# Optimization experiments

Measured on AMD Instinct MI355X. Metric: run time of the kernel, lower is better.

Reference implementation:

```python
import jax, jax.numpy as jnp
import numpy as np

RADIUS = 4.0

def _gather(x, idx):
    # x: [b, C, N], idx: [b, n, k] -> out: [b, C, k, n]
    b, C, N = x.shape
    _, n, k = idx.shape
    idxT = jnp.broadcast_to(idx.transpose(0, 2, 1)[:, None, :, :], (b, C, k, n))
    return jnp.take_along_axis(x[:, :, None, :], idxT, axis=3)


def setup_inputs() -> dict:
    key = jax.random.key(0)
    k1, k2, k3, k4, k5, k6 = jax.random.split(key, 6)
    b, N, k = 2, 50000, 16
    c_in, c_out, K = 64, 128, 5
    c2 = c_out // 2
    xyz = jax.random.normal(k1, (b, 3, N), dtype=jnp.float32)
    fea = jax.random.normal(k2, (b, c_in, N), dtype=jnp.float32)
    knn_idx = jax.random.randint(k3, (b, N, k), 0, N)
    conv_w = jax.random.normal(k4, (c2, c_in), dtype=jnp.float32) * 0.05
    conv_b = jax.random.normal(k5, (c2,), dtype=jnp.float32) * 0.01
    # uniform init matching torch: bound = sqrt(3)*gain/sqrt(fan), gain=sqrt(2), fan=16
    bound = float(np.sqrt(3.0) * np.sqrt(2.0) / np.sqrt(16.0))
    conv_dw = jax.random.uniform(k6, (1, c2, K, K, K), dtype=jnp.float32, minval=-bound, maxval=bound)
    return {"xyz": xyz, "fea": fea, "knn_idx": knn_idx, "conv_w": conv_w, "conv_b": conv_b, "conv_dw": conv_dw}


def reference(xyz, fea, knn_idx, conv_w, conv_b, conv_dw):
    b, n, k = knn_idx.shape
    K = conv_dw.shape[-1]
    # --- geometry: gather neighbor coords, relative coords, normalize ---
    neighbor_xyz = _gather(xyz, knn_idx)            # [b, 3, k, n]
    rel = neighbor_xyz - xyz[:, :, None, :]         # [b, 3, k, n]
    std = jnp.std(rel, axis=(2, 3), keepdims=True, ddof=1)  # torch unbiased std
    sample = rel / (RADIUS * std)                   # normalized grid coords in channel dim
    # --- features: residual gather (center + neighbor diffs), 1x1 conv ---
    center = fea[:, :, None, :]                     # [b, C, 1, n]
    nb = _gather(fea, knn_idx[:, :, 1:])            # [b, C, k-1, n]
    nfea = jnp.concatenate([center, nb - center], axis=2)  # [b, C, k, n]
    nfea = jnp.einsum('oc,bckn->bokn', conv_w, nfea) + conv_b[None, :, None, None]
    # --- grid_sample(mode='nearest', padding='border', align_corners=False) ---
    def to_idx(coord):
        ix = ((coord + 1.0) * K - 1.0) * 0.5
        return jnp.clip(jnp.round(ix), 0, K - 1).astype(jnp.int32)
    ix = to_idx(sample[:, 0])  # grid x -> W index, [b, k, n]
    iy = to_idx(sample[:, 1])  # grid y -> H index
    iz = to_idx(sample[:, 2])  # grid z -> D index
    kern = conv_dw[0][:, iz, iy, ix]                # [C2, b, k, n]
    kern = jnp.transpose(kern, (1, 0, 2, 3))        # [b, C2, k, n]
    # --- weighted reduce over neighbors + mean branch ---
    out = jnp.concatenate([(kern * nfea).sum(axis=2), nfea.mean(axis=2)], axis=1)
    return out  # [b, out_channels, n]
```

## Files before the change

### kernel.cpp

```cpp
#include <hip/hip_runtime.h>
#include <hip/hip_bf16.h>
#include <math.h>

#define NPTS 50000
#define BATCH 2
#define CIN 64
#define C2 64
#define KNN 16
#define NCELL 125
#define MTOT 800000


using bf16x8 = __attribute__((ext_vector_type(8))) short;
using f32x4  = __attribute__((ext_vector_type(4))) float;
using f32x2  = __attribute__((ext_vector_type(2))) float;

__device__ __forceinline__ f32x2 unpk(unsigned int v) {
    f32x2 r;
    r.x = __uint_as_float(v << 16);
    r.y = __uint_as_float(v & 0xffff0000u);
    return r;
}
__device__ __forceinline__ unsigned short f2bf(float f) {
    __hip_bfloat16 h = __float2bfloat16(f);
    return *(unsigned short*)&h;
}

__device__ __forceinline__ int to_cell32(float s) {
    float x = __fmul_rn(__fsub_rn(__fmul_rn(__fadd_rn(s, 1.0f), 5.0f), 1.0f), 0.5f);
    x = rintf(x);
    x = fminf(fmaxf(x, 0.0f), 4.0f);
    return (int)x;
}

__device__ __forceinline__ void leafwalk(int l, int& off, int& n) {
    off = 0; n = 25000;
    #pragma unroll
    for (int d = 7; d >= 0; --d) {
        int n2 = (n >> 1); n2 -= (n2 & 7);
        if ((l >> d) & 1) { off += n2; n -= n2; } else { n = n2; }
    }
}

__global__ __launch_bounds__(256) void kprep(const float* __restrict__ xyz,
                                             const float* __restrict__ dw,
                                             float* __restrict__ wsf) {
    int bx = blockIdx.x;
    int t = threadIdx.x;
    if (bx < 391) {
        int gid = bx * 256 + t;
        if (gid < 2 * NPTS) {
            int b = (gid >= NPTS);
            int n = gid - b * NPTS;
            const float* xb = xyz + (size_t)b * 3 * NPTS;
            float3 v;
            v.x = xb[n]; v.y = xb[NPTS + n]; v.z = xb[2 * NPTS + n];
            ((float3*)(wsf + 16384))[gid] = v;
        }
    } else {
        unsigned int* gdwp = (unsigned int*)(wsf + 8192);
        int i0 = (bx - 391) * 250;
        for (int i = i0 + t; i < i0 + 250; i += 256) {
            int cell = i >> 5, u = i & 31;
            unsigned int p0 = f2bf(dw[(2 * u)     * NCELL + cell]);
            unsigned int p1 = f2bf(dw[(2 * u + 1) * NCELL + cell]);
            gdwp[i] = p0 | (p1 << 16);
        }
    }
}

__global__ __launch_bounds__(256) void kfuse1(const int* __restrict__ knn,
                                              const float* __restrict__ fea,
                                              const float* __restrict__ W,
                                              unsigned short* __restrict__ g,
                                              float3* __restrict__ rel3,
                                              float* __restrict__ wsf) {
    __shared__ unsigned short flds[64 * 72];
    int bx = blockIdx.x;
    int t = threadIdx.x;
    if (bx < 1564) {
        int b = (bx >= 782);
        int tile = bx - b * 782;
        int n0 = tile * 64;
        int nrem = NPTS - n0; if (nrem > 64) nrem = 64;
        const float* fb = fea + (size_t)b * CIN * NPTS;
        int j = t & 63, w = t >> 6;
        int lane = t & 63, li = lane & 15, gq = lane >> 4;
        #pragma unroll
        for (int i = 0; i < 8; ++i) {
            int c = w * 2 + i * 8;
            float v0 = (j < nrem) ? fb[(size_t)c * NPTS + n0 + j] : 0.0f;
            float v1 = (j < nrem) ? fb[(size_t)(c + 1) * NPTS + n0 + j] : 0.0f;
            unsigned int pk = (unsigned int)f2bf(v0) | ((unsigned int)f2bf(v1) << 16);
            *(unsigned int*)&flds[j * 72 + c] = pk;
        }
        bf16x8 af[4][2];
        #pragma unroll
        for (int mt = 0; mt < 4; ++mt)
            #pragma unroll
            for (int kh = 0; kh < 2; ++kh) {
                const float* wp = W + (mt * 16 + li) * CIN + kh * 32 + gq * 8;
                float4 wa = *(const float4*)wp;
                float4 wb = *(const float4*)(wp + 4);
                bf16x8 a;
                a[0] = (short)f2bf(wa.x); a[1] = (short)f2bf(wa.y);
                a[2] = (short)f2bf(wa.z); a[3] = (short)f2bf(wa.w);
                a[4] = (short)f2bf(wb.x); a[5] = (short)f2bf(wb.y);
                a[6] = (short)f2bf(wb.z); a[7] = (short)f2bf(wb.w);
                af[mt][kh] = a;
            }
        __syncthreads();
        f32x4 acc[4];
        #pragma unroll
        for (int mt = 0; mt < 4; ++mt) acc[mt] = (f32x4){0.f, 0.f, 0.f, 0.f};
        #pragma unroll
        for (int kh = 0; kh < 2; ++kh) {
            bf16x8 bfv = *(const bf16x8*)&flds[(w * 16 + li) * 72 + kh * 32 + gq * 8];
            #pragma unroll
            for (int mt = 0; mt < 4; ++mt)
                acc[mt] = __builtin_amdgcn_mfma_f32_16x16x32_bf16(af[mt][kh], bfv,
                                                                  acc[mt], 0, 0, 0);
        }
        int nloc = w * 16 + li;
        if (nloc < nrem) {
            unsigned short* gr = g + ((size_t)b * NPTS + n0 + nloc) * C2;
            #pragma unroll
            for (int mt = 0; mt < 4; ++mt) {
                int ob = mt * 16 + gq * 4;
                uint2 pk;
                pk.x = (unsigned int)f2bf(acc[mt][0]) | ((unsigned int)f2bf(acc[mt][1]) << 16);
                pk.y = (unsigned int)f2bf(acc[mt][2]) | ((unsigned int)f2bf(acc[mt][3]) << 16);
                *(uint2*)(gr + ob) = pk;
            }
        }
    } else {
        float* lsum = (float*)flds;
        const float3* xyzT = (const float3*)(wsf + 16384);
        int pid = bx - 1564;
        int b = pid >> 8, r8 = pid & 255;
        int s = r8 >> 3, blk = r8 & 7;
        const float3* xT = xyzT + (size_t)b * NPTS;
        const int* kb = knn + (size_t)b * NPTS * KNN;
        float3* relb = rel3 + (size_t)b * MTOT;
        int l = blk * 32 + (t >> 3);
        int j = t & 7;
        int off, n;
        leafwalk(l, off, n);
        int base = s * 25000 + off;
        float r0 = 0.0f, r1 = 0.0f, r2 = 0.0f;
        int i = j;
        for (; i + 24 < n; i += 32) {
            int f0 = base + i, f1 = f0 + 8, f2 = f0 + 16, f3 = f0 + 24;
            int kk0 = f0 / NPTS, nn0 = f0 - kk0 * NPTS;
            int kk1 = f1 / NPTS, nn1 = f1 - kk1 * NPTS;
            int kk2 = f2 / NPTS, nn2 = f2 - kk2 * NPTS;
            int kk3 = f3 / NPTS, nn3 = f3 - kk3 * NPTS;
            int jA = kb[nn0 * KNN + kk0];
            int jB = kb[nn1 * KNN + kk1];
            int jC = kb[nn2 * KNN + kk2];
            int jD = kb[nn3 * KNN + kk3];
            float3 cA = xT[nn0], nA = xT[jA];
            float3 cB = xT[nn1], nB = xT[jB];
            float3 cC = xT[nn2], nC = xT[jC];
            float3 cD = xT[nn3], nD = xT[jD];
            float3 vA, vB, vC, vD;
            vA.x = __fsub_rn(nA.x, cA.x); vA.y = __fsub_rn(nA.y, cA.y); vA.z = __fsub_rn(nA.z, cA.z);
            vB.x = __fsub_rn(nB.x, cB.x); vB.y = __fsub_rn(nB.y, cB.y); vB.z = __fsub_rn(nB.z, cB.z);
            vC.x = __fsub_rn(nC.x, cC.x); vC.y = __fsub_rn(nC.y, cC.y); vC.z = __fsub_rn(nC.z, cC.z);
            vD.x = __fsub_rn(nD.x, cD.x); vD.y = __fsub_rn(nD.y, cD.y); vD.z = __fsub_rn(nD.z, cD.z);
            relb[f0] = vA; relb[f1] = vB; relb[f2] = vC; relb[f3] = vD;
            r0 = __fadd_rn(r0, vA.x); r1 = __fadd_rn(r1, vA.y); r2 = __fadd_rn(r2, vA.z);
            r0 = __fadd_rn(r0, vB.x); r1 = __fadd_rn(r1, vB.y); r2 = __fadd_rn(r2, vB.z);
            r0 = __fadd_rn(r0, vC.x); r1 = __fadd_rn(r1, vC.y); r2 = __fadd_rn(r2, vC.z);
            r0 = __fadd_rn(r0, vD.x); r1 = __fadd_rn(r1, vD.y); r2 = __fadd_rn(r2, vD.z);
        }
        for (; i < n; i += 8) {
            int f = base + i;
            int kk = f / NPTS, nn = f - kk * NPTS;
            int jj = kb[nn * KNN + kk];
            float3 cc = xT[nn], nv = xT[jj];
            float3 v;
            v.x = __fsub_rn(nv.x, cc.x); v.y = __fsub_rn(nv.y, cc.y); v.z = __fsub_rn(nv.z, cc.z);
            relb[f] = v;
            r0 = __fadd_rn(r0, v.x); r1 = __fadd_rn(r1, v.y); r2 = __fadd_rn(r2, v.z);
        }
        float a0 = __fadd_rn(r0, __shfl_xor(r0, 1));
        a0 = __fadd_rn(a0, __shfl_xor(a0, 2));
        a0 = __fadd_rn(a0, __shfl_xor(a0, 4));
        float a1 = __fadd_rn(r1, __shfl_xor(r1, 1));
        a1 = __fadd_rn(a1, __shfl_xor(a1, 2));
        a1 = __fadd_rn(a1, __shfl_xor(a1, 4));
        float a2 = __fadd_rn(r2, __shfl_xor(r2, 1));
        a2 = __fadd_rn(a2, __shfl_xor(a2, 2));
        a2 = __fadd_rn(a2, __shfl_xor(a2, 4));
        #pragma unroll
        for (int c = 0; c < 3; ++c) {
            float rc = (c == 0) ? a0 : ((c == 1) ? a1 : a2);
            __syncthreads();
            if (j == 0) lsum[t >> 3] = rc;
            __syncthreads();
            for (int m = 16; m >= 1; m >>= 1) {
                float v = 0.0f;
                if (t < m) v = __fadd_rn(lsum[2 * t], lsum[2 * t + 1]);
                __syncthreads();
                if (t < m) lsum[t] = v;
                __syncthreads();
            }
            if (t == 0) wsf[16 + ((size_t)(b * 3 + c) * 32 + s) * 8 + blk] = lsum[0];
        }
    }
}

__global__ __launch_bounds__(256) void kpw2(const float3* __restrict__ rel3,
                                            float* __restrict__ wsf) {
    __shared__ float sm[96];
    int r8 = blockIdx.x;
    int s = r8 >> 3, blk = r8 & 7;
    int b = blockIdx.y;
    int t = threadIdx.x;

    if (t < 96) {
        int c = t >> 5, l = t & 31;
        const float* q = wsf + 16 + (size_t)(b * 3 + c) * 256 + l * 8;
        float a  = __fadd_rn(__fadd_rn(q[0], q[1]), __fadd_rn(q[2], q[3]));
        float b2 = __fadd_rn(__fadd_rn(q[4], q[5]), __fadd_rn(q[6], q[7]));
        sm[c * 32 + l] = __fadd_rn(a, b2);
    }
    __syncthreads();
    for (int m = 16; m >= 1; m >>= 1) {
        float v = 0.0f;
        int c = t >> 5, l = t & 31;
        if (t < 96 && l < m) v = __fadd_rn(sm[c * 32 + 2 * l], sm[c * 32 + 2 * l + 1]);
        __syncthreads();
        if (t < 96 && l < m) sm[c * 32 + l] = v;
        __syncthreads();
    }
    float m0 = sm[0]  / 800000.0f;
    float m1 = sm[32] / 800000.0f;
    float m2 = sm[64] / 800000.0f;
    __syncthreads();

    const float3* relb = rel3 + (size_t)b * MTOT;
    int l = blk * 32 + (t >> 3);
    int j = t & 7;
    int off, n;
    leafwalk(l, off, n);
    int base = s * 25000 + off;
    float r0 = 0.0f, r1 = 0.0f, r2 = 0.0f;
    int i = j;
    for (; i + 24 < n; i += 32) {
        float3 vA = relb[base + i];
        float3 vB = relb[base + i + 8];
        float3 vC = relb[base + i + 16];
        float3 vD = relb[base + i + 24];
        float dA0 = __fsub_rn(vA.x, m0), dA1 = __fsub_rn(vA.y, m1), dA2 = __fsub_rn(vA.z, m2);
        float dB0 = __fsub_rn(vB.x, m0), dB1 = __fsub_rn(vB.y, m1), dB2 = __fsub_rn(vB.z, m2);
        float dC0 = __fsub_rn(vC.x, m0), dC1 = __fsub_rn(vC.y, m1), dC2 = __fsub_rn(vC.z, m2);
        float dD0 = __fsub_rn(vD.x, m0), dD1 = __fsub_rn(vD.y, m1), dD2 = __fsub_rn(vD.z, m2);
        r0 = __fadd_rn(r0, __fmul_rn(dA0, dA0));
        r1 = __fadd_rn(r1, __fmul_rn(dA1, dA1));
        r2 = __fadd_rn(r2, __fmul_rn(dA2, dA2));
        r0 = __fadd_rn(r0, __fmul_rn(dB0, dB0));
        r1 = __fadd_rn(r1, __fmul_rn(dB1, dB1));
        r2 = __fadd_rn(r2, __fmul_rn(dB2, dB2));
        r0 = __fadd_rn(r0, __fmul_rn(dC0, dC0));
        r1 = __fadd_rn(r1, __fmul_rn(dC1, dC1));
        r2 = __fadd_rn(r2, __fmul_rn(dC2, dC2));
        r0 = __fadd_rn(r0, __fmul_rn(dD0, dD0));
        r1 = __fadd_rn(r1, __fmul_rn(dD1, dD1));
        r2 = __fadd_rn(r2, __fmul_rn(dD2, dD2));
    }
    for (; i < n; i += 8) {
        float3 v = relb[base + i];
        float d0 = __fsub_rn(v.x, m0), d1 = __fsub_rn(v.y, m1), d2 = __fsub_rn(v.z, m2);
        r0 = __fadd_rn(r0, __fmul_rn(d0, d0));
        r1 = __fadd_rn(r1, __fmul_rn(d1, d1));
        r2 = __fadd_rn(r2, __fmul_rn(d2, d2));
    }
    float a0 = __fadd_rn(r0, __shfl_xor(r0, 1));
    a0 = __fadd_rn(a0, __shfl_xor(a0, 2));
    a0 = __fadd_rn(a0, __shfl_xor(a0, 4));
    float a1 = __fadd_rn(r1, __shfl_xor(r1, 1));
    a1 = __fadd_rn(a1, __shfl_xor(a1, 2));
    a1 = __fadd_rn(a1, __shfl_xor(a1, 4));
    float a2 = __fadd_rn(r2, __shfl_xor(r2, 1));
    a2 = __fadd_rn(a2, __shfl_xor(a2, 2));
    a2 = __fadd_rn(a2, __shfl_xor(a2, 4));
    #pragma unroll
    for (int c = 0; c < 3; ++c) {
        float rc = (c == 0) ? a0 : ((c == 1) ? a1 : a2);
        __syncthreads();
        if (j == 0) sm[t >> 3] = rc;
        __syncthreads();
        for (int m = 16; m >= 1; m >>= 1) {
            float v = 0.0f;
            if (t < m) v = __fadd_rn(sm[2 * t], sm[2 * t + 1]);
            __syncthreads();
            if (t < m) sm[t] = v;
            __syncthreads();
        }
        if (t == 0) wsf[2048 + ((size_t)(b * 3 + c) * 32 + s) * 8 + blk] = sm[0];
    }
}

__global__ __launch_bounds__(256, 6) void kmain(const int* __restrict__ idx,
                                                const float* __restrict__ cb,
                                                const unsigned short* __restrict__ g,
                                                const float* __restrict__ wsf,
                                                float* __restrict__ out) {
    __shared__ unsigned int  dwp[NCELL * 32];
    __shared__ unsigned char celllds[64 * KNN];
    __shared__ float         ctr[3][64];
    __shared__ float         res[128 * 17];
    int bx = blockIdx.x;
    int sub = bx & 7;
    int b = sub >> 2;
    int tile = (bx >> 3) * 4 + (sub & 3);
    if (tile >= 782) return;
    int n0 = tile * 64;
    int t = threadIdx.x;
    int nrem = NPTS - n0; if (nrem > 64) nrem = 64;

    float* l3 = res;
    if (t < 96) {
        int c = t >> 5, l = t & 31;
        const float* q = wsf + 2048 + (size_t)(b * 3 + c) * 256 + l * 8;
        float a  = __fadd_rn(__fadd_rn(q[0], q[1]), __fadd_rn(q[2], q[3]));
        float b2 = __fadd_rn(__fadd_rn(q[4], q[5]), __fadd_rn(q[6], q[7]));
        l3[c * 32 + l] = __fadd_rn(a, b2);
    }
    __syncthreads();
    for (int m = 16; m >= 1; m >>= 1) {
        float v = 0.0f;
        int c = t >> 5, l = t & 31;
        if (t < 96 && l < m) v = __fadd_rn(l3[c * 32 + 2 * l], l3[c * 32 + 2 * l + 1]);
        __syncthreads();
        if (t < 96 && l < m) l3[c * 32 + l] = v;
        __syncthreads();
    }
    float dn0 = __fmul_rn(4.0f, sqrtf(l3[0]  / 799999.0f));
    float dn1 = __fmul_rn(4.0f, sqrtf(l3[32] / 799999.0f));
    float dn2 = __fmul_rn(4.0f, sqrtf(l3[64] / 799999.0f));
    __syncthreads();

    const unsigned int* gdwp = (const unsigned int*)(wsf + 8192);
    for (int i = t; i < NCELL * 32; i += 256) dwp[i] = gdwp[i];
    const float3* xT = (const float3*)(wsf + 16384) + (size_t)b * NPTS;
    if (t < 64) {
        if (t < nrem) {
            float3 v = xT[n0 + t];
            ctr[0][t] = v.x; ctr[1][t] = v.y; ctr[2][t] = v.z;
        }
    }
    const int* ib = idx + ((size_t)b * NPTS + n0) * KNN;
    __syncthreads();

    for (int i = t; i < nrem * KNN; i += 256) {
        int p = i >> 4;
        int jx = ib[i];
        float3 pj = xT[jx];
        float sx = __fsub_rn(pj.x, ctr[0][p]) / dn0;
        float sy = __fsub_rn(pj.y, ctr[1][p]) / dn1;
        float sz = __fsub_rn(pj.z, ctr[2][p]) / dn2;
        celllds[i] = (unsigned char)((to_cell32(sz) * 5 + to_cell32(sy)) * 5 + to_cell32(sx));
    }
    __syncthreads();

    int w = t >> 6, h = (t >> 5) & 1, u = t & 31;
    int o0 = 2 * u, o1 = 2 * u + 1;
    f32x2 cbv;
    cbv.x = cb[o0]; cbv.y = cb[o1];
    const unsigned short* gbp = g + (size_t)b * NPTS * C2;
    float* ob = out + (size_t)b * 128 * NPTS;

    #pragma unroll 1
    for (int chunk = 0; chunk < 4; ++chunk) {
        int pbase = chunk * 16;
        #pragma unroll 1
        for (int i = 0; i < 2; ++i) {
            int p = pbase + i * 8 + w * 2 + h;
            if (p < nrem) {
                const int* row = ib + p * KNN;
                unsigned int gnu = *(const unsigned int*)(gbp + (size_t)(n0 + p) * C2 + o0);
                unsigned int gvv[15];
                #pragma unroll
                for (int k = 0; k < 15; ++k) {
                    int jj = row[k + 1];
                    gvv[k] = *(const unsigned int*)(gbp + (size_t)jj * C2 + o0);
                }
                int cell0 = celllds[p * KNN];
                f32x2 k0v = unpk(dwp[cell0 * 32 + u]);
                f32x2 gn  = unpk(gnu);
                f32x2 ws = {0.f, 0.f}, gs = {0.f, 0.f}, sk = {0.f, 0.f};
                #pragma unroll
                for (int k = 0; k < 15; ++k) {
                    int cell = celllds[p * KNN + k + 1];
                    f32x2 dp = unpk(dwp[cell * 32 + u]);
                    f32x2 gv = unpk(gvv[k]);
                    ws += dp * gv;
                    gs += gv;
                    sk += dp;
                }
                f32x2 r1 = cbv * (k0v + sk) + gn * (k0v - sk) + ws;
                f32x2 r2 = cbv + 0.0625f * (gs - 14.0f * gn);
                int pl = p & 15;
                res[o0 * 17 + pl]        = r1.x;
                res[o1 * 17 + pl]        = r1.y;
                res[(64 + o0) * 17 + pl] = r2.x;
                res[(64 + o1) * 17 + pl] = r2.y;
            }
        }
        __syncthreads();
        int rl = t >> 4;
        int jn = t & 15;
        int ncol = nrem - pbase; if (ncol > 16) ncol = 16;
        if (jn < ncol) {
            for (int r2 = rl; r2 < 128; r2 += 16)
                ob[(size_t)r2 * NPTS + n0 + pbase + jn] = res[r2 * 17 + jn];
        }
        __syncthreads();
    }
}

extern "C" void kernel_launch(void* const* d_in, const int* in_sizes, int n_in,
                              void* d_out, int out_size, void* d_ws, size_t ws_size,
                              hipStream_t stream) {
    const float* xyz   = (const float*)d_in[0];
    const float* fea   = (const float*)d_in[1];
    const int*   knn   = (const int*)d_in[2];
    const float* convw = (const float*)d_in[3];
    const float* convb = (const float*)d_in[4];
    const float* convdw= (const float*)d_in[5];
    float* out = (float*)d_out;
    float* wsf = (float*)d_ws;
    unsigned short* g = (unsigned short*)(wsf + 327680);
    float3* rel3 = (float3*)out;

    kprep <<<407, 256, 0, stream>>>(xyz, convdw, wsf);
    kfuse1<<<1564 + 512, 256, 0, stream>>>(knn, fea, convw, g, rel3, wsf);
    kpw2  <<<dim3(256, BATCH), 256, 0, stream>>>(rel3, wsf);
    kmain <<<1568, 256, 0, stream>>>(knn, convb, g, wsf, out);
}
```

Measured before the change: 99.51 us.

## Split cell computation into separate kernel and halve channels per main block

Moves the per-neighbor grid-cell index computation out of the main kernel into a new kcell kernel that writes byte cell indices to workspace. The main kernel now splits the 64 output channels into two halves across blocks, so each block stages half the depthwise weight table in LDS and holds a smaller result buffer, allowing higher occupancy (launch bound 8) and twice as many blocks. Each block processes four points per wave per chunk instead of two serial iterations, and output writes use nontemporal stores. The cost is an extra kernel launch, a global round-trip for the cell bytes, and the knn index rows being read twice, once by each half.

New measurement: 103.9 us. 4.4% more time.

```diff
diff --git a/kernel.cpp b/kernel.cpp
--- a/kernel.cpp
+++ b/kernel.cpp
@@ -303,25 +303,16 @@
     }
 }
 
-__global__ __launch_bounds__(256, 6) void kmain(const int* __restrict__ idx,
-                                                const float* __restrict__ cb,
-                                                const unsigned short* __restrict__ g,
-                                                const float* __restrict__ wsf,
-                                                float* __restrict__ out) {
-    __shared__ unsigned int  dwp[NCELL * 32];
-    __shared__ unsigned char celllds[64 * KNN];
-    __shared__ float         ctr[3][64];
-    __shared__ float         res[128 * 17];
-    int bx = blockIdx.x;
-    int sub = bx & 7;
-    int b = sub >> 2;
-    int tile = (bx >> 3) * 4 + (sub & 3);
-    if (tile >= 782) return;
+__global__ __launch_bounds__(256) void kcell(const int* __restrict__ idx,
+                                             const float* __restrict__ wsf,
+                                             unsigned char* __restrict__ cells) {
+    __shared__ float l3[96];
+    __shared__ float ctr[3][64];
+    int tile = blockIdx.x, b = blockIdx.y;
     int n0 = tile * 64;
     int t = threadIdx.x;
     int nrem = NPTS - n0; if (nrem > 64) nrem = 64;
 
-    float* l3 = res;
     if (t < 96) {
         int c = t >> 5, l = t & 31;
         const float* q = wsf + 2048 + (size_t)(b * 3 + c) * 256 + l * 8;
@@ -341,20 +332,16 @@
     float dn0 = __fmul_rn(4.0f, sqrtf(l3[0]  / 799999.0f));
     float dn1 = __fmul_rn(4.0f, sqrtf(l3[32] / 799999.0f));
     float dn2 = __fmul_rn(4.0f, sqrtf(l3[64] / 799999.0f));
-    __syncthreads();
-
-    const unsigned int* gdwp = (const unsigned int*)(wsf + 8192);
-    for (int i = t; i < NCELL * 32; i += 256) dwp[i] = gdwp[i];
+
     const float3* xT = (const float3*)(wsf + 16384) + (size_t)b * NPTS;
-    if (t < 64) {
-        if (t < nrem) {
-            float3 v = xT[n0 + t];
-            ctr[0][t] = v.x; ctr[1][t] = v.y; ctr[2][t] = v.z;
-        }
+    if (t < 64 && t < nrem) {
+        float3 v = xT[n0 + t];
+        ctr[0][t] = v.x; ctr[1][t] = v.y; ctr[2][t] = v.z;
     }
     const int* ib = idx + ((size_t)b * NPTS + n0) * KNN;
     __syncthreads();
 
+    unsigned char* cw = cells + ((size_t)b * NPTS + n0) * KNN;
     for (int i = t; i < nrem * KNN; i += 256) {
         int p = i >> 4;
         int jx = ib[i];
@@ -362,61 +349,90 @@
         float sx = __fsub_rn(pj.x, ctr[0][p]) / dn0;
         float sy = __fsub_rn(pj.y, ctr[1][p]) / dn1;
         float sz = __fsub_rn(pj.z, ctr[2][p]) / dn2;
-        celllds[i] = (unsigned char)((to_cell32(sz) * 5 + to_cell32(sy)) * 5 + to_cell32(sx));
-    }
+        cw[i] = (unsigned char)((to_cell32(sz) * 5 + to_cell32(sy)) * 5 + to_cell32(sx));
+    }
+}
+
+__global__ __launch_bounds__(256, 8) void kmain2(const int* __restrict__ idx,
+                                                 const float* __restrict__ cb,
+                                                 const unsigned short* __restrict__ g,
+                                                 const unsigned char* __restrict__ cells,
+                                                 const float* __restrict__ wsf,
+                                                 float* __restrict__ out) {
+    __shared__ unsigned int  dwph[NCELL * 16];
+    __shared__ unsigned char celllds[64 * KNN];
+    __shared__ float         res[64 * 17];
+    int bx = blockIdx.x;
+    int sub = bx & 7;
+    int part = sub & 3;
+    int half = part >> 1, b = part & 1;
+    int tile = (bx >> 3) * 2 + (sub >> 2);
+    if (tile >= 782) return;
+    int n0 = tile * 64;
+    int t = threadIdx.x;
+    int nrem = NPTS - n0; if (nrem > 64) nrem = 64;
+
+    const unsigned int* gdwp = (const unsigned int*)(wsf + 8192);
+    for (int i = t; i < NCELL * 16; i += 256) {
+        int cell = i >> 4, u = i & 15;
+        dwph[i] = gdwp[cell * 32 + half * 16 + u];
+    }
+    const unsigned char* cr = cells + ((size_t)b * NPTS + n0) * KNN;
+    int nb = (nrem * KNN) >> 2;
+    if (t < nb) ((unsigned int*)celllds)[t] = ((const unsigned int*)cr)[t];
+    const int* ib = idx + ((size_t)b * NPTS + n0) * KNN;
     __syncthreads();
 
-    int w = t >> 6, h = (t >> 5) & 1, u = t & 31;
-    int o0 = 2 * u, o1 = 2 * u + 1;
+    int w = t >> 6, lane = t & 63, u = lane & 15, pg = lane >> 4;
     f32x2 cbv;
-    cbv.x = cb[o0]; cbv.y = cb[o1];
-    const unsigned short* gbp = g + (size_t)b * NPTS * C2;
+    cbv.x = cb[half * 32 + 2 * u]; cbv.y = cb[half * 32 + 2 * u + 1];
+    const unsigned short* gbp = g + (size_t)b * NPTS * C2 + half * 32;
     float* ob = out + (size_t)b * 128 * NPTS;
 
     #pragma unroll 1
     for (int chunk = 0; chunk < 4; ++chunk) {
-        int pbase = chunk * 16;
-        #pragma unroll 1
-        for (int i = 0; i < 2; ++i) {
-            int p = pbase + i * 8 + w * 2 + h;
-            if (p < nrem) {
-                const int* row = ib + p * KNN;
-                unsigned int gnu = *(const unsigned int*)(gbp + (size_t)(n0 + p) * C2 + o0);
-                unsigned int gvv[15];
-                #pragma unroll
-                for (int k = 0; k < 15; ++k) {
-                    int jj = row[k + 1];
-                    gvv[k] = *(const unsigned int*)(gbp + (size_t)jj * C2 + o0);
-                }
-                int cell0 = celllds[p * KNN];
-                f32x2 k0v = unpk(dwp[cell0 * 32 + u]);
-                f32x2 gn  = unpk(gnu);
-                f32x2 ws = {0.f, 0.f}, gs = {0.f, 0.f}, sk = {0.f, 0.f};
-                #pragma unroll
-                for (int k = 0; k < 15; ++k) {
-                    int cell = celllds[p * KNN + k + 1];
-                    f32x2 dp = unpk(dwp[cell * 32 + u]);
-                    f32x2 gv = unpk(gvv[k]);
-                    ws += dp * gv;
-                    gs += gv;
-                    sk += dp;
-                }
-                f32x2 r1 = cbv * (k0v + sk) + gn * (k0v - sk) + ws;
-                f32x2 r2 = cbv + 0.0625f * (gs - 14.0f * gn);
-                int pl = p & 15;
-                res[o0 * 17 + pl]        = r1.x;
-                res[o1 * 17 + pl]        = r1.y;
-                res[(64 + o0) * 17 + pl] = r2.x;
-                res[(64 + o1) * 17 + pl] = r2.y;
-            }
+        int p = chunk * 16 + w * 4 + pg;
+        if (p < nrem) {
+            const int* row = ib + p * KNN;
+            unsigned int gnu = *(const unsigned int*)(gbp + (size_t)(n0 + p) * C2 + 2 * u);
+            unsigned int gvv[15];
+            #pragma unroll
+            for (int k = 0; k < 15; ++k) {
+                int jj = row[k + 1];
+                gvv[k] = *(const unsigned int*)(gbp + (size_t)jj * C2 + 2 * u);
+            }
+            int cell0 = celllds[p * KNN];
+            f32x2 k0v = unpk(dwph[cell0 * 16 + u]);
+            f32x2 gn  = unpk(gnu);
+            f32x2 ws = {0.f, 0.f}, gs = {0.f, 0.f}, sk = {0.f, 0.f};
+            #pragma unroll
+            for (int k = 0; k < 15; ++k) {
+                int cell = celllds[p * KNN + k + 1];
+                f32x2 dp = unpk(dwph[cell * 16 + u]);
+                f32x2 gv = unpk(gvv[k]);
+                ws += dp * gv;
+                gs += gv;
+                sk += dp;
+            }
+            f32x2 r1 = cbv * (k0v + sk) + gn * (k0v - sk) + ws;
+            f32x2 r2 = cbv + 0.0625f * (gs - 14.0f * gn);
+            int pl = p & 15;
+            res[(2 * u)      * 17 + pl] = r1.x;
+            res[(2 * u + 1)  * 17 + pl] = r1.y;
+            res[(32 + 2 * u) * 17 + pl] = r2.x;
+            res[(33 + 2 * u) * 17 + pl] = r2.y;
         }
         __syncthreads();
         int rl = t >> 4;
         int jn = t & 15;
+        int pbase = chunk * 16;
         int ncol = nrem - pbase; if (ncol > 16) ncol = 16;
         if (jn < ncol) {
-            for (int r2 = rl; r2 < 128; r2 += 16)
-                ob[(size_t)r2 * NPTS + n0 + pbase + jn] = res[r2 * 17 + jn];
+            for (int r2i = rl; r2i < 64; r2i += 16) {
+                int grow = (r2i < 32) ? (half * 32 + r2i) : (64 + half * 32 + (r2i - 32));
+                __builtin_nontemporal_store(res[r2i * 17 + jn],
+                                            &ob[(size_t)grow * NPTS + n0 + pbase + jn]);
+            }
         }
         __syncthreads();
     }
@@ -434,10 +450,12 @@
     float* out = (float*)d_out;
     float* wsf = (float*)d_ws;
     unsigned short* g = (unsigned short*)(wsf + 327680);
+    unsigned char* cells = (unsigned char*)(g + (size_t)BATCH * NPTS * C2);
     float3* rel3 = (float3*)out;
 
     kprep <<<407, 256, 0, stream>>>(xyz, convdw, wsf);
     kfuse1<<<1564 + 512, 256, 0, stream>>>(knn, fea, convw, g, rel3, wsf);
     kpw2  <<<dim3(256, BATCH), 256, 0, stream>>>(rel3, wsf);
-    kmain <<<1568, 256, 0, stream>>>(knn, convb, g, wsf, out);
-}
+    kcell <<<dim3(782, BATCH), 256, 0, stream>>>(knn, wsf, cells);
+    kmain2<<<782 * 4, 256, 0, stream>>>(knn, convb, g, cells, wsf, out);
+}
```
